# Kernel tuning notes

Measured on AMD Instinct MI355X. Metric: run time of the kernel, lower is better.

## Reference

```python
import jax, jax.numpy as jnp
import numpy as np
import math

D_MODEL = 96
D_STATE = 16
IMG = 32
KSZ = 3
V_LIST = [(0, 0), (0, 1), (0, -1), (1, 0), (-1, 0)]
NUM_V = len(V_LIST)
GROUPS = 4
BATCH = 4


def group_norm(x, gamma, beta, groups=GROUPS, eps=1e-5):
    B, C, H, W = x.shape
    xg = x.reshape(B, groups, C // groups, H, W)
    mu = xg.mean(axis=(2, 3, 4), keepdims=True)
    var = xg.var(axis=(2, 3, 4), keepdims=True)
    xn = ((xg - mu) * jax.lax.rsqrt(var + eps)).reshape(B, C, H, W)
    return xn * gamma[None, :, None, None] + beta[None, :, None, None]


def circ_conv(x, w, b=None):
    # circular padding then VALID conv == padding_mode='circular'
    p = w.shape[-1] // 2
    xp = jnp.pad(x, ((0, 0), (0, 0), (p, p), (p, p)), mode='wrap')
    y = jax.lax.conv_general_dilated(xp, w, (1, 1), 'VALID',
                                     dimension_numbers=('NCHW', 'OIHW', 'NCHW'))
    if b is not None:
        y = y + b[None, :, None, None]
    return y


def setup_inputs() -> dict:
    key = jax.random.key(0)
    ks = jax.random.split(key, 8)
    fan = D_MODEL * KSZ * KSZ
    inp = {
        'u_t': jax.random.normal(ks[0], (BATCH, D_MODEL, IMG, IMG), jnp.float32),
        's_prev': jax.random.normal(ks[1], (BATCH, NUM_V, D_MODEL, D_STATE, IMG, IMG), jnp.float32) * 0.1,
        'gamma': jnp.ones((D_MODEL,), jnp.float32),
        'beta': jnp.zeros((D_MODEL,), jnp.float32),
        'w_delta': jax.random.normal(ks[2], (D_MODEL, D_MODEL, KSZ, KSZ), jnp.float32) / np.sqrt(fan),
        'b_delta': jnp.zeros((D_MODEL,), jnp.float32),
        'w_B': jax.random.normal(ks[3], (D_STATE, D_MODEL, KSZ, KSZ), jnp.float32) / np.sqrt(fan),
        'w_C': jax.random.normal(ks[4], (D_STATE, D_MODEL, KSZ, KSZ), jnp.float32) / np.sqrt(fan),
        'log_A_real': jnp.full((D_MODEL, D_STATE), math.log(0.5), jnp.float32),
        'D_param': jnp.ones((D_MODEL,), jnp.float32),
        'dt_inv_softplus': jnp.asarray(math.log(math.exp(1.0) - 1.0), jnp.float32),
    }
    return inp


def reference(u_t, s_prev, gamma, beta, w_delta, b_delta, w_B, w_C, log_A_real, D_param, dt_inv_softplus):
    B, D, H, W = u_t.shape
    N = D_STATE
    u_norm = group_norm(u_t, gamma, beta)
    delta = jax.nn.softplus(circ_conv(u_norm, w_delta, b_delta) + dt_inv_softplus)
    delta = jnp.clip(delta, 1e-4, 5.0)                          # (B,D,H,W)
    B_val = circ_conv(u_norm, w_B)                               # (B,N,H,W)
    C_val = circ_conv(u_norm, w_C)                               # (B,N,H,W)
    A = -jnp.exp(log_A_real)                                     # (D,N)
    delta_bc = delta[:, :, None]                                 # (B,D,1,H,W)
    A_bar = jnp.exp(delta_bc * A[None, :, :, None, None])        # (B,D,N,H,W)
    B_bar = delta_bc * B_val[:, None]                            # (B,D,N,H,W)
    # flow transport: dest[y,x] = src[(y-vy)%H,(x-vx)%W] == roll by (vy,vx)
    s_tr = jnp.stack([jnp.roll(s_prev[:, i], shift=v, axis=(-2, -1))
                      for i, v in enumerate(V_LIST)], axis=1)    # (B,V,D,N,H,W)
    s_new = A_bar[:, None] * s_tr + B_bar[:, None] * u_t[:, None, :, None]
    y_state = jnp.sum(s_new * C_val[:, None, None], axis=3)      # (B,V,D,H,W)
    y_out = y_state + u_t[:, None] * D_param[None, None, :, None, None]
    return (y_out, s_new)
```

## Files before the change

kernel.cpp:

```cpp
#include <hip/hip_runtime.h>
#include <math.h>

#define D_MODEL 96
#define D_STATE 16
#define IMG 32
#define NUM_V 5
#define GROUPS 4
#define BATCH 4
#define HW (IMG*IMG)
#define CPG (D_MODEL/GROUPS)
#define NCOEF (D_MODEL + 2*D_STATE)
#define Y_SIZE (BATCH*NUM_V*D_MODEL*HW)

typedef float f32x4 __attribute__((ext_vector_type(4)));

__device__ __forceinline__ void nt_store4(const float4& v, float4* p) {
    f32x4 tmp = {v.x, v.y, v.z, v.w};
    __builtin_nontemporal_store(tmp, (f32x4*)p);
}

__global__ __launch_bounds__(256) void gn_kernel(const float4* __restrict__ u4,
                                                 const float* __restrict__ gamma,
                                                 const float* __restrict__ beta,
                                                 float4* __restrict__ unorm4) {
    int b = blockIdx.x >> 2, g = blockIdx.x & 3;
    int t = threadIdx.x;
    const int base4 = ((b * D_MODEL + g * CPG) * HW) >> 2;
    const int n4 = (CPG * HW) >> 2;
    float s = 0.f, s2 = 0.f;
    for (int k = t; k < n4; k += 256) {
        float4 v = u4[base4 + k];
        s += v.x + v.y + v.z + v.w;
        s2 = fmaf(v.x, v.x, fmaf(v.y, v.y, fmaf(v.z, v.z, fmaf(v.w, v.w, s2))));
    }
    for (int off = 32; off; off >>= 1) {
        s  += __shfl_down(s,  off);
        s2 += __shfl_down(s2, off);
    }
    __shared__ float red[8];
    int wid = t >> 6;
    if ((t & 63) == 0) { red[wid * 2] = s; red[wid * 2 + 1] = s2; }
    __syncthreads();
    if (t == 0) {
        float S = 0.f, S2 = 0.f;
        for (int i = 0; i < 4; ++i) { S += red[i * 2]; S2 += red[i * 2 + 1]; }
        float nf = (float)(CPG * HW);
        float mu  = S / nf;
        float var = S2 / nf - mu * mu;
        red[0] = mu;
        red[1] = rsqrtf(var + 1e-5f);
    }
    __syncthreads();
    float mu = red[0], rs = red[1];
    for (int k = t; k < n4; k += 256) {
        int c = g * CPG + (k >> 8);
        float ga = gamma[c] * rs, be = beta[c] - mu * gamma[c] * rs;
        float4 v = u4[base4 + k];
        float4 o;
        o.x = fmaf(v.x, ga, be); o.y = fmaf(v.y, ga, be);
        o.z = fmaf(v.z, ga, be); o.w = fmaf(v.w, ga, be);
        unorm4[base4 + k] = o;
    }
}

__global__ __launch_bounds__(256) void conv_kernel(const float4* __restrict__ unorm4,
                                                   const float* __restrict__ w_delta,
                                                   const float* __restrict__ b_delta,
                                                   const float* __restrict__ w_B,
                                                   const float* __restrict__ w_C,
                                                   const float* __restrict__ dt_ptr,
                                                   float4* __restrict__ coef4) {
    int bid = blockIdx.x;
    int b  = bid >> 7;
    int oc = bid & 127;
    int t  = threadIdx.x;
    int h  = t >> 3;
    int j  = t & 7;
    int lane = t & 63;
    int ll = (lane & 56) | ((j + 7) & 7);
    int rl = (lane & 56) | ((j + 1) & 7);

    const float* wp;
    float bias;
    bool is_delta = false;
    if (oc < D_MODEL) {
        wp = w_delta + oc * D_MODEL * 9;
        bias = b_delta[oc] + dt_ptr[0];
        is_delta = true;
    } else if (oc < D_MODEL + D_STATE) {
        wp = w_B + (oc - D_MODEL) * D_MODEL * 9;
        bias = 0.f;
    } else {
        wp = w_C + (oc - D_MODEL - D_STATE) * D_MODEL * 9;
        bias = 0.f;
    }
    const float4* ub4 = unorm4 + ((b * D_MODEL * HW) >> 2);

    float4 acc = {bias, bias, bias, bias};
    int hm = (h + 31) & 31, hp = (h + 1) & 31;
    int ro[3] = {hm * 8 + j, h * 8 + j, hp * 8 + j};

    for (int ic = 0; ic < D_MODEL; ++ic) {
        const float* wr = wp + ic * 9;
        const int icb = ic * 256;
        #pragma unroll
        for (int kh = 0; kh < 3; ++kh) {
            float4 q = ub4[icb + ro[kh]];
            float lw = __shfl(q.w, ll);
            float rx = __shfl(q.x, rl);
            float wa = wr[kh * 3 + 0], wb = wr[kh * 3 + 1], wc = wr[kh * 3 + 2];
            acc.x = fmaf(wa, lw,  fmaf(wb, q.x, fmaf(wc, q.y, acc.x)));
            acc.y = fmaf(wa, q.x, fmaf(wb, q.y, fmaf(wc, q.z, acc.y)));
            acc.z = fmaf(wa, q.y, fmaf(wb, q.z, fmaf(wc, q.w, acc.z)));
            acc.w = fmaf(wa, q.z, fmaf(wb, q.w, fmaf(wc, rx,  acc.w)));
        }
    }
    if (is_delta) {
        float* a = (float*)&acc;
        #pragma unroll
        for (int k = 0; k < 4; ++k) {
            float x = a[k];
            float sp = x > 20.f ? x : log1pf(__expf(x));
            a[k] = fminf(fmaxf(sp, 1e-4f), 5.f);
        }
    }
    coef4[((b * NCOEF + oc) * HW >> 2) + h * 8 + j] = acc;
}

__global__ __launch_bounds__(256) void state_kernel(const float4* __restrict__ u4,
                                                    const float4* __restrict__ s_prev4,
                                                    const float4* __restrict__ coef4,
                                                    const float* __restrict__ log_A,
                                                    const float* __restrict__ D_param,
                                                    float4* __restrict__ out4) {
    int bid = blockIdx.x;
    int b = bid / (NUM_V * D_MODEL);
    int r = bid - b * (NUM_V * D_MODEL);
    int i = r / D_MODEL;
    int d = r - i * D_MODEL;

    int t = threadIdx.x;
    int h = t >> 3;
    int j = t & 7;
    int lane = t & 63;
    int ll = (lane & 56) | ((j + 7) & 7);
    int rl = (lane & 56) | ((j + 1) & 7);
    int hw4 = t;

    int src4 = hw4;
    if (i == 3) src4 = (((h + 31) & 31) << 3) | j;
    if (i == 4) src4 = (((h + 1) & 31) << 3) | j;
    const int mode = (i == 1) ? 1 : (i == 2) ? 2 : 0;

    float4 delta = coef4[((b * NCOEF + d) * HW >> 2) + hw4];
    float4 u     = u4[((b * D_MODEL + d) * HW >> 2) + hw4];
    float Dp     = D_param[d];
    const float* lA = log_A + d * D_STATE;

    const long pb = (long)((b * NUM_V + i) * D_MODEL + d) * (D_STATE * HW / 4);
    const float4* sp = s_prev4 + pb;
    float4* outs = out4 + (Y_SIZE >> 2) + pb;
    const float4* Bp = coef4 + ((b * NCOEF + D_MODEL) * HW >> 2) + hw4;
    const float4* Cp = coef4 + ((b * NCOEF + D_MODEL + D_STATE) * HW >> 2) + hw4;

    float4 y = {0.f, 0.f, 0.f, 0.f};

    #pragma unroll 4
    for (int n = 0; n < D_STATE; ++n) {
        int n4 = n * (HW / 4);
        float4 Bv = Bp[n4];
        float4 Cv = Cp[n4];
        float4 q  = sp[n4 + src4];
        float A = -__expf(lA[n]);
        float4 Ab, bu;
        Ab.x = __expf(delta.x * A); Ab.y = __expf(delta.y * A);
        Ab.z = __expf(delta.z * A); Ab.w = __expf(delta.w * A);
        bu.x = delta.x * Bv.x * u.x; bu.y = delta.y * Bv.y * u.y;
        bu.z = delta.z * Bv.z * u.z; bu.w = delta.w * Bv.w * u.w;

        float4 s = q;
        if (mode == 1) {
            float lw = __shfl(q.w, ll);
            s.x = lw; s.y = q.x; s.z = q.y; s.w = q.z;
        } else if (mode == 2) {
            float rx = __shfl(q.x, rl);
            s.x = q.y; s.y = q.z; s.z = q.w; s.w = rx;
        }

        float4 sn;
        sn.x = fmaf(Ab.x, s.x, bu.x); sn.y = fmaf(Ab.y, s.y, bu.y);
        sn.z = fmaf(Ab.z, s.z, bu.z); sn.w = fmaf(Ab.w, s.w, bu.w);
        nt_store4(sn, &outs[n4 + hw4]);
        y.x = fmaf(sn.x, Cv.x, y.x); y.y = fmaf(sn.y, Cv.y, y.y);
        y.z = fmaf(sn.z, Cv.z, y.z); y.w = fmaf(sn.w, Cv.w, y.w);
    }

    float4 o;
    o.x = fmaf(u.x, Dp, y.x); o.y = fmaf(u.y, Dp, y.y);
    o.z = fmaf(u.z, Dp, y.z); o.w = fmaf(u.w, Dp, y.w);
    out4[(((b * NUM_V + i) * D_MODEL + d) * HW >> 2) + hw4] = o;
}

extern "C" void kernel_launch(void* const* d_in, const int* in_sizes, int n_in,
                              void* d_out, int out_size, void* d_ws, size_t ws_size,
                              hipStream_t stream) {
    const float* u_t     = (const float*)d_in[0];
    const float* s_prev  = (const float*)d_in[1];
    const float* gamma   = (const float*)d_in[2];
    const float* beta    = (const float*)d_in[3];
    const float* w_delta = (const float*)d_in[4];
    const float* b_delta = (const float*)d_in[5];
    const float* w_B     = (const float*)d_in[6];
    const float* w_C     = (const float*)d_in[7];
    const float* log_A   = (const float*)d_in[8];
    const float* D_param = (const float*)d_in[9];
    const float* dt_ptr  = (const float*)d_in[10];
    float* out = (float*)d_out;

    float* unorm = (float*)d_ws;
    float* coef  = unorm + BATCH * D_MODEL * HW;

    hipLaunchKernelGGL(gn_kernel, dim3(BATCH * GROUPS), dim3(256), 0, stream,
                       (const float4*)u_t, gamma, beta, (float4*)unorm);
    hipLaunchKernelGGL(conv_kernel, dim3(BATCH * NCOEF), dim3(256), 0, stream,
                       (const float4*)unorm, w_delta, b_delta, w_B, w_C, dt_ptr,
                       (float4*)coef);
    hipLaunchKernelGGL(state_kernel, dim3(BATCH * NUM_V * D_MODEL), dim3(256), 0, stream,
                       (const float4*)u_t, (const float4*)s_prev, (const float4*)coef,
                       log_A, D_param, (float4*)out);
}
```

Before: 316.3 us.

## Share A_bar/B_bar across flow directions in state kernel, split image in halves

The state kernel now makes one block handle all five flow directions for a given (batch, channel) and half of the image. A_bar and B*delta*u are computed once per state index and reused across the five directions instead of being recomputed per direction. Loads are batched eight states at a time to raise memory-level parallelism. The grid shrinks from 1920 blocks of 256 threads to 768 blocks of 128 threads. That lowers parallelism and raises register pressure from the per-direction arrays on a kernel that is mostly memory-bound.

```diff
diff --git a/kernel.cpp b/kernel.cpp
--- a/kernel.cpp
+++ b/kernel.cpp
@@ -127,78 +127,107 @@
     coef4[((b * NCOEF + oc) * HW >> 2) + h * 8 + j] = acc;
 }
 
-__global__ __launch_bounds__(256) void state_kernel(const float4* __restrict__ u4,
-                                                    const float4* __restrict__ s_prev4,
-                                                    const float4* __restrict__ coef4,
-                                                    const float* __restrict__ log_A,
-                                                    const float* __restrict__ D_param,
-                                                    float4* __restrict__ out4) {
-    int bid = blockIdx.x;
-    int b = bid / (NUM_V * D_MODEL);
-    int r = bid - b * (NUM_V * D_MODEL);
-    int i = r / D_MODEL;
-    int d = r - i * D_MODEL;
-
-    int t = threadIdx.x;
-    int h = t >> 3;
-    int j = t & 7;
+__global__ __launch_bounds__(128, 2) void state_kernel(const float4* __restrict__ u4,
+                                                       const float4* __restrict__ s_prev4,
+                                                       const float4* __restrict__ coef4,
+                                                       const float* __restrict__ log_A,
+                                                       const float* __restrict__ D_param,
+                                                       float4* __restrict__ out4) {
+    int bid  = blockIdx.x;
+    int half = bid & 1;
+    int bd   = bid >> 1;
+    int b = bd / D_MODEL;
+    int d = bd - b * D_MODEL;
+
+    int t   = threadIdx.x;
+    int hw4 = half * 128 + t;
+    int h   = hw4 >> 3;
+    int j   = t & 7;
     int lane = t & 63;
     int ll = (lane & 56) | ((j + 7) & 7);
     int rl = (lane & 56) | ((j + 1) & 7);
-    int hw4 = t;
-
-    int src4 = hw4;
-    if (i == 3) src4 = (((h + 31) & 31) << 3) | j;
-    if (i == 4) src4 = (((h + 1) & 31) << 3) | j;
-    const int mode = (i == 1) ? 1 : (i == 2) ? 2 : 0;
-
-    float4 delta = coef4[((b * NCOEF + d) * HW >> 2) + hw4];
-    float4 u     = u4[((b * D_MODEL + d) * HW >> 2) + hw4];
+    int up4 = (((h + 31) & 31) << 3) | j;
+    int dn4 = (((h + 1) & 31) << 3) | j;
+
+    float4 delta = coef4[(b * NCOEF + d) * 256 + hw4];
+    float4 u     = u4[(b * D_MODEL + d) * 256 + hw4];
     float Dp     = D_param[d];
     const float* lA = log_A + d * D_STATE;
 
-    const long pb = (long)((b * NUM_V + i) * D_MODEL + d) * (D_STATE * HW / 4);
-    const float4* sp = s_prev4 + pb;
-    float4* outs = out4 + (Y_SIZE >> 2) + pb;
-    const float4* Bp = coef4 + ((b * NCOEF + D_MODEL) * HW >> 2) + hw4;
-    const float4* Cp = coef4 + ((b * NCOEF + D_MODEL + D_STATE) * HW >> 2) + hw4;
-
-    float4 y = {0.f, 0.f, 0.f, 0.f};
-
-    #pragma unroll 4
-    for (int n = 0; n < D_STATE; ++n) {
-        int n4 = n * (HW / 4);
-        float4 Bv = Bp[n4];
-        float4 Cv = Cp[n4];
-        float4 q  = sp[n4 + src4];
-        float A = -__expf(lA[n]);
-        float4 Ab, bu;
-        Ab.x = __expf(delta.x * A); Ab.y = __expf(delta.y * A);
-        Ab.z = __expf(delta.z * A); Ab.w = __expf(delta.w * A);
-        bu.x = delta.x * Bv.x * u.x; bu.y = delta.y * Bv.y * u.y;
-        bu.z = delta.z * Bv.z * u.z; bu.w = delta.w * Bv.w * u.w;
-
-        float4 s = q;
-        if (mode == 1) {
-            float lw = __shfl(q.w, ll);
-            s.x = lw; s.y = q.x; s.z = q.y; s.w = q.z;
-        } else if (mode == 2) {
-            float rx = __shfl(q.x, rl);
-            s.x = q.y; s.y = q.z; s.z = q.w; s.w = rx;
-        }
-
-        float4 sn;
-        sn.x = fmaf(Ab.x, s.x, bu.x); sn.y = fmaf(Ab.y, s.y, bu.y);
-        sn.z = fmaf(Ab.z, s.z, bu.z); sn.w = fmaf(Ab.w, s.w, bu.w);
-        nt_store4(sn, &outs[n4 + hw4]);
-        y.x = fmaf(sn.x, Cv.x, y.x); y.y = fmaf(sn.y, Cv.y, y.y);
-        y.z = fmaf(sn.z, Cv.z, y.z); y.w = fmaf(sn.w, Cv.w, y.w);
-    }
-
-    float4 o;
-    o.x = fmaf(u.x, Dp, y.x); o.y = fmaf(u.y, Dp, y.y);
-    o.z = fmaf(u.z, Dp, y.z); o.w = fmaf(u.w, Dp, y.w);
-    out4[(((b * NUM_V + i) * D_MODEL + d) * HW >> 2) + hw4] = o;
+    const float4* Bp = coef4 + (b * NCOEF + D_MODEL) * 256 + hw4;
+    const float4* Cp = coef4 + (b * NCOEF + D_MODEL + D_STATE) * 256 + hw4;
+
+    long sbase[NUM_V];
+    #pragma unroll
+    for (int i = 0; i < NUM_V; ++i)
+        sbase[i] = (long)((b * NUM_V + i) * D_MODEL + d) * (D_STATE * 256);
+
+    float4* outs = out4 + (Y_SIZE >> 2);
+    float4 y[NUM_V];
+    #pragma unroll
+    for (int i = 0; i < NUM_V; ++i) y[i] = (float4){0.f, 0.f, 0.f, 0.f};
+
+    #pragma unroll
+    for (int c = 0; c < 2; ++c) {
+        const int n0 = c * 8;
+        float4 Ab[8], bu[8];
+        #pragma unroll
+        for (int k = 0; k < 8; ++k) {
+            float4 Bv = Bp[(n0 + k) * 256];
+            float A = -__expf(lA[n0 + k]);
+            Ab[k].x = __expf(delta.x * A); Ab[k].y = __expf(delta.y * A);
+            Ab[k].z = __expf(delta.z * A); Ab[k].w = __expf(delta.w * A);
+            bu[k].x = delta.x * Bv.x * u.x; bu[k].y = delta.y * Bv.y * u.y;
+            bu[k].z = delta.z * Bv.z * u.z; bu[k].w = delta.w * Bv.w * u.w;
+        }
+        #pragma unroll
+        for (int i = 0; i < NUM_V; ++i) {
+            const int src = (i == 3) ? up4 : (i == 4) ? dn4 : hw4;
+            const float4* spb = s_prev4 + sbase[i];
+            float4* so = outs + sbase[i];
+            float4 s[8], Cv[8];
+            #pragma unroll
+            for (int k = 0; k < 8; ++k) s[k]  = spb[(n0 + k) * 256 + src];
+            #pragma unroll
+            for (int k = 0; k < 8; ++k) Cv[k] = Cp[(n0 + k) * 256];
+            if (i == 1) {
+                #pragma unroll
+                for (int k = 0; k < 8; ++k) {
+                    float lw = __shfl(s[k].w, ll);
+                    float4 q = s[k];
+                    s[k].x = lw; s[k].y = q.x; s[k].z = q.y; s[k].w = q.z;
+                }
+            } else if (i == 2) {
+                #pragma unroll
+                for (int k = 0; k < 8; ++k) {
+                    float rx = __shfl(s[k].x, rl);
+                    float4 q = s[k];
+                    s[k].x = q.y; s[k].y = q.z; s[k].z = q.w; s[k].w = rx;
+                }
+            }
+            #pragma unroll
+            for (int k = 0; k < 8; ++k) {
+                float4 sn;
+                sn.x = fmaf(Ab[k].x, s[k].x, bu[k].x);
+                sn.y = fmaf(Ab[k].y, s[k].y, bu[k].y);
+                sn.z = fmaf(Ab[k].z, s[k].z, bu[k].z);
+                sn.w = fmaf(Ab[k].w, s[k].w, bu[k].w);
+                nt_store4(sn, &so[(n0 + k) * 256 + hw4]);
+                y[i].x = fmaf(sn.x, Cv[k].x, y[i].x);
+                y[i].y = fmaf(sn.y, Cv[k].y, y[i].y);
+                y[i].z = fmaf(sn.z, Cv[k].z, y[i].z);
+                y[i].w = fmaf(sn.w, Cv[k].w, y[i].w);
+            }
+        }
+    }
+
+    #pragma unroll
+    for (int i = 0; i < NUM_V; ++i) {
+        float4 o;
+        o.x = fmaf(u.x, Dp, y[i].x); o.y = fmaf(u.y, Dp, y[i].y);
+        o.z = fmaf(u.z, Dp, y[i].z); o.w = fmaf(u.w, Dp, y[i].w);
+        out4[((b * NUM_V + i) * D_MODEL + d) * 256 + hw4] = o;
+    }
 }
 
 extern "C" void kernel_launch(void* const* d_in, const int* in_sizes, int n_in,
@@ -225,7 +254,7 @@
     hipLaunchKernelGGL(conv_kernel, dim3(BATCH * NCOEF), dim3(256), 0, stream,
                        (const float4*)unorm, w_delta, b_delta, w_B, w_C, dt_ptr,
                        (float4*)coef);
-    hipLaunchKernelGGL(state_kernel, dim3(BATCH * NUM_V * D_MODEL), dim3(256), 0, stream,
+    hipLaunchKernelGGL(state_kernel, dim3(BATCH * D_MODEL * 2), dim3(128), 0, stream,
                        (const float4*)u_t, (const float4*)s_prev, (const float4*)coef,
                        log_A, D_param, (float4*)out);
 }
```

After: 312.2 us. About the same (-1.3%).
